# Kernel optimization log

Hardware: AMD Instinct MI355X
Metric: run time of the kernel (lower is better)

Reference implementation:

```python
import jax, jax.numpy as jnp
import numpy as np
from jax import lax

B, S, I, H, L = 128, 256, 64, 128, 64
N_SUB = 2  # fixed RK4 substeps per observation interval (replaces adaptive dopri5)


def setup_inputs() -> dict:
    key = jax.random.key(0)
    ks = jax.random.split(key, 16)
    sc = 0.05
    x = jax.random.normal(ks[0], (B, S, I), jnp.float32)
    # strictly increasing irregular observation times
    times = jnp.sort(jax.random.uniform(ks[1], (S,), jnp.float32) * 10.0)
    return {
        "x": x,
        "times": times,
        "W_ih": jax.random.normal(ks[2], (3 * H, I), jnp.float32) * sc,
        "W_hh": jax.random.normal(ks[3], (3 * H, H), jnp.float32) * sc,
        "b_ih": jnp.zeros((3 * H,), jnp.float32),
        "b_hh": jnp.zeros((3 * H,), jnp.float32),
        "ode_W1": jax.random.normal(ks[4], (H, H), jnp.float32) * sc,
        "ode_b1": jnp.zeros((H,), jnp.float32),
        "ode_W2": jax.random.normal(ks[5], (H, H), jnp.float32) * sc,
        "ode_b2": jnp.zeros((H,), jnp.float32),
        "W_mean": jax.random.normal(ks[6], (L, H), jnp.float32) * sc,
        "b_mean": jnp.zeros((L,), jnp.float32),
        "W_logvar": jax.random.normal(ks[7], (L, H), jnp.float32) * sc,
        "b_logvar": jnp.zeros((L,), jnp.float32),
    }


def reference(x, times, W_ih, W_hh, b_ih, b_hh, ode_W1, ode_b1, ode_W2, ode_b2,
              W_mean, b_mean, W_logvar, b_logvar):
    def ode_f(h):  # MLP dynamics: Linear -> tanh -> Linear (time-independent)
        return jnp.tanh(h @ ode_W1.T + ode_b1) @ ode_W2.T + ode_b2

    def rk4(h, dt):
        k1 = ode_f(h)
        k2 = ode_f(h + 0.5 * dt * k1)
        k3 = ode_f(h + 0.5 * dt * k2)
        k4 = ode_f(h + dt * k3)
        return h + (dt / 6.0) * (k1 + 2.0 * k2 + 2.0 * k3 + k4)

    def gru(x_t, h):  # torch.nn.GRUCell math
        gx = x_t @ W_ih.T + b_ih
        gh = h @ W_hh.T + b_hh
        rx, zx, nx = jnp.split(gx, 3, axis=-1)
        rh, zh, nh = jnp.split(gh, 3, axis=-1)
        r = jax.nn.sigmoid(rx + rh)
        z = jax.nn.sigmoid(zx + zh)
        n = jnp.tanh(nx + r * nh)
        return (1.0 - z) * n + z * h

    # iterate i = S-1 .. 0; before each GRU update (except the first, i=S-1)
    # evolve h from t_{i+1} backward to t_i  -> dt_i = t_i - t_{i+1} (negative)
    dt_rev = jnp.concatenate([jnp.zeros((1,), times.dtype),
                              (times[:-1] - times[1:])[::-1]])  # [S]
    x_rev = jnp.transpose(x[:, ::-1, :], (1, 0, 2))  # [S, B, I]

    def step(h, inp):
        x_t, dt = inp
        sub = dt / N_SUB
        for _ in range(N_SUB):  # fixed small unroll
            h = rk4(h, sub)
        h = gru(x_t, h)
        return h, None

    h0 = jnp.zeros((x.shape[0], W_hh.shape[1]), x.dtype)
    h, _ = lax.scan(step, h0, (x_rev, dt_rev))
    mean = h @ W_mean.T + b_mean
    logvar = h @ W_logvar.T + b_logvar
    return (mean, logvar)
```

## Files before the change

### kernel.cpp

```cpp
#include <hip/hip_runtime.h>

#define NB 128
#define NS 256
#define NI 64
#define NH 128
#define NL 64
#define NG 384

typedef _Float16 f16;
typedef __attribute__((ext_vector_type(2))) _Float16 f16x2;

__device__ __forceinline__ float fast_tanh(float x) {
    float e = __expf(2.0f * x);
    return 1.0f - 2.0f / (e + 1.0f);
}
__device__ __forceinline__ float fast_sig(float x) {
    return 1.0f / (1.0f + __expf(-x));
}
__device__ __forceinline__ float red1(float a) {
    int ai = __builtin_bit_cast(int, a);
    int bi = __builtin_amdgcn_update_dpp(0, ai, 0xB1, 0xF, 0xF, true);
    return a + __builtin_bit_cast(float, bi);
}
__device__ __forceinline__ float fdot2(f16x2 a, f16x2 b, float c) {
#if __has_builtin(__builtin_amdgcn_fdot2)
    return __builtin_amdgcn_fdot2(a, b, c, false);
#else
    return c + (float)a.x * (float)b.x + (float)a.y * (float)b.y;
#endif
}
__device__ __forceinline__ f16x2 bc16(unsigned int u) {
    return __builtin_bit_cast(f16x2, u);
}
__device__ __forceinline__ void sync_lds() {
    asm volatile("s_waitcnt lgkmcnt(0)" ::: "memory");
    __builtin_amdgcn_s_barrier();
    asm volatile("" ::: "memory");
}

__device__ __align__(16) f16 g_W1h[NH * NH];
__device__ __align__(16) f16 g_W2h[NH * NH];
__device__ __align__(16) f16 g_W12h[NH * NH];
__device__ __align__(16) f16 g_Whhh[3 * NH * NH];
__device__ __align__(16) f16 g_Whh2h[3 * NH * NH];
__device__ float g_w1b2[NH];
__device__ float g_whhb2[3 * NH];

__global__ __launch_bounds__(384)
void gx_kernel(const float* __restrict__ x, const float* __restrict__ W_ih,
               const float* __restrict__ b_ih, float* __restrict__ gx)
{
    const int s = blockIdx.x;
    const int j = threadIdx.x;
    __shared__ __align__(16) float xs[NB * NI];
    for (int idx = j; idx < NB * NI; idx += 384) {
        int bb = idx >> 6, cc = idx & 63;
        xs[idx] = x[(bb * NS + s) * NI + cc];
    }
    float w[64];
#pragma unroll
    for (int c = 0; c < 64; c += 4)
        *(float4*)&w[c] = *(const float4*)&W_ih[j * NI + c];
    const float bj = b_ih[j];
    __syncthreads();
    for (int bb = 0; bb < NB; bb++) {
        const float* xr = xs + bb * NI;
        float a0 = 0.f, a1 = 0.f, a2 = 0.f, a3 = 0.f;
#pragma unroll
        for (int c = 0; c < 64; c += 4) {
            a0 = fmaf(w[c + 0], xr[c + 0], a0);
            a1 = fmaf(w[c + 1], xr[c + 1], a1);
            a2 = fmaf(w[c + 2], xr[c + 2], a2);
            a3 = fmaf(w[c + 3], xr[c + 3], a3);
        }
        gx[((size_t)s * NB + bb) * NG + j] = ((a0 + a1) + (a2 + a3)) + bj;
    }
}

__global__ __launch_bounds__(128)
void prep_kernel(const float* __restrict__ W1, const float* __restrict__ Whh,
                 const float* __restrict__ W2, const float* __restrict__ b2)
{
    const int i = blockIdx.x;
    const int j = threadIdx.x;
    __shared__ float rowA[NH];
    __shared__ float red[NH];
    const float* src = (i < NH) ? (W1 + i * NH) : (Whh + (size_t)(i - NH) * NH);
    rowA[j] = src[j];
    __syncthreads();
    float acc = 0.f;
    for (int k = 0; k < NH; k++) acc = fmaf(rowA[k], W2[k * NH + j], acc);
    if (i < NH) {
        g_W12h[i * NH + j] = (f16)acc;
        g_W1h[i * NH + j]  = (f16)rowA[j];
        g_W2h[i * NH + j]  = (f16)W2[i * NH + j];
    } else {
        g_Whh2h[(size_t)(i - NH) * NH + j] = (f16)acc;
        g_Whhh[(size_t)(i - NH) * NH + j]  = (f16)rowA[j];
    }
    red[j] = rowA[j] * b2[j];
    __syncthreads();
    for (int off = 64; off > 0; off >>= 1) {
        if (j < off) red[j] += red[j + off];
        __syncthreads();
    }
    if (j == 0) {
        if (i < NH) g_w1b2[i] = red[0];
        else        g_whhb2[i - NH] = red[0];
    }
}

#define DOT1(W, SRC, OUT)                                                      \
    {                                                                          \
        float a0_ = 0.f, a1_ = 0.f, a2_ = 0.f, a3_ = 0.f;                      \
        _Pragma("unroll") for (int j = 0; j < 8; j++)                          \
        {                                                                      \
            uint4 v_ = *(const uint4*)((const unsigned char*)(SRC) + pbase + 16 * j); \
            a0_ = fdot2(W[4 * j + 0], bc16(v_.x), a0_);                        \
            a1_ = fdot2(W[4 * j + 1], bc16(v_.y), a1_);                        \
            a2_ = fdot2(W[4 * j + 2], bc16(v_.z), a2_);                        \
            a3_ = fdot2(W[4 * j + 3], bc16(v_.w), a3_);                        \
        }                                                                      \
        OUT = red1((a0_ + a1_) + (a2_ + a3_));                                 \
    }

#define DOT2S(WA, WB, SRC, OA, OB)                                             \
    {                                                                          \
        float a0_ = 0.f, a1_ = 0.f, a2_ = 0.f, a3_ = 0.f;                      \
        float b0_ = 0.f, b1_ = 0.f, b2_ = 0.f, b3_ = 0.f;                      \
        _Pragma("unroll") for (int j = 0; j < 8; j++)                          \
        {                                                                      \
            uint4 v_ = *(const uint4*)((const unsigned char*)(SRC) + pbase + 16 * j); \
            a0_ = fdot2(WA[4 * j + 0], bc16(v_.x), a0_);                       \
            a1_ = fdot2(WA[4 * j + 1], bc16(v_.y), a1_);                       \
            a2_ = fdot2(WA[4 * j + 2], bc16(v_.z), a2_);                       \
            a3_ = fdot2(WA[4 * j + 3], bc16(v_.w), a3_);                       \
            b0_ = fdot2(WB[4 * j + 0], bc16(v_.x), b0_);                       \
            b1_ = fdot2(WB[4 * j + 1], bc16(v_.y), b1_);                       \
            b2_ = fdot2(WB[4 * j + 2], bc16(v_.z), b2_);                       \
            b3_ = fdot2(WB[4 * j + 3], bc16(v_.w), b3_);                       \
        }                                                                      \
        OA = red1((a0_ + a1_) + (a2_ + a3_));                                  \
        OB = red1((b0_ + b1_) + (b2_ + b3_));                                  \
    }

#define DOT2D(WA, SA, WB, SB, OA, OB)                                          \
    {                                                                          \
        float a0_ = 0.f, a1_ = 0.f, a2_ = 0.f, a3_ = 0.f;                      \
        float b0_ = 0.f, b1_ = 0.f, b2_ = 0.f, b3_ = 0.f;                      \
        _Pragma("unroll") for (int j = 0; j < 8; j++)                          \
        {                                                                      \
            uint4 v_ = *(const uint4*)((const unsigned char*)(SA) + pbase + 16 * j); \
            uint4 u_ = *(const uint4*)((const unsigned char*)(SB) + pbase + 16 * j); \
            a0_ = fdot2(WA[4 * j + 0], bc16(v_.x), a0_);                       \
            a1_ = fdot2(WA[4 * j + 1], bc16(v_.y), a1_);                       \
            a2_ = fdot2(WA[4 * j + 2], bc16(v_.z), a2_);                       \
            a3_ = fdot2(WA[4 * j + 3], bc16(v_.w), a3_);                       \
            b0_ = fdot2(WB[4 * j + 0], bc16(u_.x), b0_);                       \
            b1_ = fdot2(WB[4 * j + 1], bc16(u_.y), b1_);                       \
            b2_ = fdot2(WB[4 * j + 2], bc16(u_.z), b2_);                       \
            b3_ = fdot2(WB[4 * j + 3], bc16(u_.w), b3_);                       \
        }                                                                      \
        OA = red1((a0_ + a1_) + (a2_ + a3_));                                  \
        OB = red1((b0_ + b1_) + (b2_ + b3_));                                  \
    }

#define DOT4S(WA, WB, WC, WD, SRC, OA, OB, OC, OD)                             \
    {                                                                          \
        float a0_ = 0.f, a1_ = 0.f, b0_ = 0.f, b1_ = 0.f;                      \
        float c0_ = 0.f, c1_ = 0.f, d0_ = 0.f, d1_ = 0.f;                      \
        _Pragma("unroll") for (int j = 0; j < 8; j++)                          \
        {                                                                      \
            uint4 v_ = *(const uint4*)((const unsigned char*)(SRC) + pbase + 16 * j); \
            a0_ = fdot2(WA[4 * j + 0], bc16(v_.x), a0_);                       \
            a1_ = fdot2(WA[4 * j + 1], bc16(v_.y), a1_);                       \
            a0_ = fdot2(WA[4 * j + 2], bc16(v_.z), a0_);                       \
            a1_ = fdot2(WA[4 * j + 3], bc16(v_.w), a1_);                       \
            b0_ = fdot2(WB[4 * j + 0], bc16(v_.x), b0_);                       \
            b1_ = fdot2(WB[4 * j + 1], bc16(v_.y), b1_);                       \
            b0_ = fdot2(WB[4 * j + 2], bc16(v_.z), b0_);                       \
            b1_ = fdot2(WB[4 * j + 3], bc16(v_.w), b1_);                       \
            c0_ = fdot2(WC[4 * j + 0], bc16(v_.x), c0_);                       \
            c1_ = fdot2(WC[4 * j + 1], bc16(v_.y), c1_);                       \
            c0_ = fdot2(WC[4 * j + 2], bc16(v_.z), c0_);                       \
            c1_ = fdot2(WC[4 * j + 3], bc16(v_.w), c1_);                       \
            d0_ = fdot2(WD[4 * j + 0], bc16(v_.x), d0_);                       \
            d1_ = fdot2(WD[4 * j + 1], bc16(v_.y), d1_);                       \
            d0_ = fdot2(WD[4 * j + 2], bc16(v_.z), d0_);                       \
            d1_ = fdot2(WD[4 * j + 3], bc16(v_.w), d1_);                       \
        }                                                                      \
        OA = red1(a0_ + a1_);                                                  \
        OB = red1(b0_ + b1_);                                                  \
        OC = red1(c0_ + c1_);                                                  \
        OD = red1(d0_ + d1_);                                                  \
    }

#define LOADW(DST, BASE)                                                       \
    {                                                                          \
        _Pragma("unroll") for (int j = 0; j < 8; j++)                          \
        {                                                                      \
            uint4 v_ = *(const uint4*)((const unsigned char*)(BASE) + pbase + 16 * j); \
            DST[4 * j + 0] = bc16(v_.x); DST[4 * j + 1] = bc16(v_.y);          \
            DST[4 * j + 2] = bc16(v_.z); DST[4 * j + 3] = bc16(v_.w);          \
        }                                                                      \
    }

__global__ __launch_bounds__(256, 1)
void rnn_kernel(const float* __restrict__ times, const float* __restrict__ b_hh,
                const float* __restrict__ b1, const float* __restrict__ b2,
                const float* __restrict__ W_mean, const float* __restrict__ b_mean,
                const float* __restrict__ W_logvar, const float* __restrict__ b_logvar,
                const float* __restrict__ gx,
                const float* __restrict__ x, const float* __restrict__ W_ih,
                const float* __restrict__ b_ih,
                const int use_gx,
                float* __restrict__ out)
{
    const int b = blockIdx.x;
    const int t = threadIdx.x;
    const int r = t >> 1;
    const int p = t & 1;
    const int pbase = 128 * p;

    __shared__ __align__(16) f16 shHh[NH], shUh[NH], shAh[NH];
    __shared__ float shT[NS];
    __shared__ __align__(16) float shGX[NG], shX[NI], shHf[NH];

    f16x2 w1p[32], w2p[32], w12p[32];
    f16x2 wh0p[32], wh1p[32], wh2p[32];
    f16x2 ws0p[32], ws1p[32], ws2p[32];
    LOADW(w1p,  g_W1h  + r * NH);
    LOADW(w2p,  g_W2h  + r * NH);
    LOADW(w12p, g_W12h + r * NH);
    LOADW(wh0p, g_Whhh + (0 * NH + r) * NH);
    LOADW(wh1p, g_Whhh + (1 * NH + r) * NH);
    LOADW(wh2p, g_Whhh + (2 * NH + r) * NH);
    LOADW(ws0p, g_Whh2h + (size_t)(0 * NH + r) * NH);
    LOADW(ws1p, g_Whh2h + (size_t)(1 * NH + r) * NH);
    LOADW(ws2p, g_Whh2h + (size_t)(2 * NH + r) * NH);

    const float b1r = b1[r], b2r = b2[r];
    const float bh0 = b_hh[r], bh1 = b_hh[NH + r], bh2 = b_hh[2 * NH + r];
    const float w1b2r = g_w1b2[r];
    const float wb0 = g_whhb2[r], wb1 = g_whhb2[NH + r], wb2 = g_whhb2[2 * NH + r];

    if (t < NS) shT[t] = times[t];
    if (t < NH) shHh[t] = (f16)0.f;
    float h = 0.f;
    __syncthreads();

    float gxr = 0.f, gxz = 0.f, gxn = 0.f;
    if (use_gx) {
        const float* g = gx + ((size_t)(NS - 1) * NB + b) * NG;
        gxr = g[r]; gxz = g[NH + r]; gxn = g[2 * NH + r];
    }

    for (int si = 0; si < NS; ++si) {
        const int seq = NS - 1 - si;
        const float dt = (si == 0) ? 0.f : (shT[seq] - shT[seq + 1]);
        const float dts = 0.5f * dt;
        const float a2 = 0.5f * dts;
        const float a6 = dts * (1.f / 6.f);

        float gnr = 0.f, gnz = 0.f, gnn = 0.f;
        if (use_gx) {
            const int seqn = (seq > 0) ? (seq - 1) : 0;
            const float* g = gx + ((size_t)seqn * NB + b) * NG;
            gnr = g[r]; gnz = g[NH + r]; gnn = g[2 * NH + r];
        } else {
            if (t < NI) shX[t] = x[(b * NS + seq) * NI + t];
            __syncthreads();
            for (int idx = t; idx < NG; idx += 256) {
                const float* wr = W_ih + idx * NI;
                float a = 0.f;
#pragma unroll
                for (int cc = 0; cc < NI; cc += 4) {
                    float4 w4 = *(const float4*)(wr + cc);
                    a = fmaf(w4.x, shX[cc + 0], a);
                    a = fmaf(w4.y, shX[cc + 1], a);
                    a = fmaf(w4.z, shX[cc + 2], a);
                    a = fmaf(w4.w, shX[cc + 3], a);
                }
                shGX[idx] = a + b_ih[idx];
            }
            __syncthreads();
        }

        float z1a, u, S, m;
        DOT1(w1p, shHh, z1a);
        z1a += b1r;
        u = fast_tanh(z1a);
        if (p == 0) shUh[r] = (f16)u;
        S = u;
        sync_lds();
        DOT1(w12p, shUh, m);
        u = fast_tanh(z1a + a2 * (m + w1b2r));
        if (p == 0) shUh[r] = (f16)u;
        S += 2.f * u;
        sync_lds();
        DOT1(w12p, shUh, m);
        u = fast_tanh(z1a + a2 * (m + w1b2r));
        if (p == 0) shUh[r] = (f16)u;
        S += 2.f * u;
        sync_lds();
        DOT1(w12p, shUh, m);
        u = fast_tanh(z1a + dts * (m + w1b2r));
        S += u;
        if (p == 0) shUh[r] = (f16)S;
        sync_lds();
        float mA, mB;
        DOT2S(w2p, w12p, shUh, mA, mB);
        const float hA = h + a6 * mA + dts * b2r;
        const float z1b = z1a + a6 * mB + dts * w1b2r;
        u = fast_tanh(z1b);
        if (p == 0) { shAh[r] = (f16)hA; shUh[r] = (f16)u; }
        float S2 = u;
        sync_lds();

        float g0, g1, g2;
        DOT2D(w12p, shUh, wh0p, shAh, m, g0);
        u = fast_tanh(z1b + a2 * (m + w1b2r));
        if (p == 0) shUh[r] = (f16)u;
        S2 += 2.f * u;
        sync_lds();
        DOT2D(w12p, shUh, wh1p, shAh, m, g1);
        u = fast_tanh(z1b + a2 * (m + w1b2r));
        if (p == 0) shUh[r] = (f16)u;
        S2 += 2.f * u;
        sync_lds();
        DOT2D(w12p, shUh, wh2p, shAh, m, g2);
        u = fast_tanh(z1b + dts * (m + w1b2r));
        S2 += u;
        if (p == 0) shUh[r] = (f16)S2;
        sync_lds();
        float n0, n1, n2, n3;
        DOT4S(w2p, ws0p, ws1p, ws2p, shUh, n0, n1, n2, n3);
        const float hB = hA + a6 * n0 + dts * b2r;
        const float rh = g0 + a6 * n1 + dts * wb0 + bh0;
        const float zh = g1 + a6 * n2 + dts * wb1 + bh1;
        const float nh = g2 + a6 * n3 + dts * wb2 + bh2;
        float rx, zx, nx;
        if (use_gx) { rx = gxr; zx = gxz; nx = gxn; }
        else        { rx = shGX[r]; zx = shGX[NH + r]; nx = shGX[2 * NH + r]; }
        const float rr = fast_sig(rx + rh);
        const float zz = fast_sig(zx + zh);
        const float nn = fast_tanh(nx + rr * nh);
        h = (1.f - zz) * nn + zz * hB;
        if (p == 0) shHh[r] = (f16)h;
        gxr = gnr; gxz = gnz; gxn = gnn;
        sync_lds();
    }

    if (p == 0) shHf[r] = h;
    __syncthreads();
    const int sel = r >> 6;
    const int l = r & 63;
    const float* Wf = sel ? W_logvar : W_mean;
    const int hc0 = 64 * p;
    float a0 = 0.f, a1 = 0.f;
#pragma unroll
    for (int jj = 0; jj < 16; jj++) {
        float4 w4 = *(const float4*)&Wf[l * NH + hc0 + 4 * jj];
        float4 h4 = *(const float4*)(shHf + hc0 + 4 * jj);
        a0 = fmaf(w4.x, h4.x, a0);
        a1 = fmaf(w4.y, h4.y, a1);
        a0 = fmaf(w4.z, h4.z, a0);
        a1 = fmaf(w4.w, h4.w, a1);
    }
    float acc = red1(a0 + a1);
    if (p == 0) {
        const float bias = sel ? b_logvar[l] : b_mean[l];
        out[sel * (NB * NL) + b * NL + l] = acc + bias;
    }
}

extern "C" void kernel_launch(void* const* d_in, const int* in_sizes, int n_in,
                              void* d_out, int out_size, void* d_ws, size_t ws_size,
                              hipStream_t stream)
{
    const float* x        = (const float*)d_in[0];
    const float* times    = (const float*)d_in[1];
    const float* W_ih     = (const float*)d_in[2];
    const float* W_hh     = (const float*)d_in[3];
    const float* b_ih     = (const float*)d_in[4];
    const float* b_hh     = (const float*)d_in[5];
    const float* W1       = (const float*)d_in[6];
    const float* b1       = (const float*)d_in[7];
    const float* W2       = (const float*)d_in[8];
    const float* b2       = (const float*)d_in[9];
    const float* W_mean   = (const float*)d_in[10];
    const float* b_mean   = (const float*)d_in[11];
    const float* W_logvar = (const float*)d_in[12];
    const float* b_logvar = (const float*)d_in[13];
    float* out = (float*)d_out;

    float* gxbuf = (float*)d_ws;
    const size_t need = (size_t)NS * NB * NG * sizeof(float);
    const int use_gx = (d_ws != nullptr && ws_size >= need) ? 1 : 0;

    if (use_gx) {
        gx_kernel<<<NS, 384, 0, stream>>>(x, W_ih, b_ih, gxbuf);
    }
    prep_kernel<<<512, 128, 0, stream>>>(W1, W_hh, W2, b2);
    rnn_kernel<<<NB, 256, 0, stream>>>(times, b_hh, b1, b2,
                                       W_mean, b_mean, W_logvar, b_logvar,
                                       gxbuf, x, W_ih, b_ih, use_gx, out);
}
```

Before: 917.8 us.

## Warp-specialize RNN kernel with readlane broadcast matvecs instead of LDS exchanges

Restructures the per-batch recurrent kernel so one wavefront owns the entire ODE MLP chain, with each lane holding two full rows of the weights. The hidden and intermediate vectors are packed as f16 pairs and broadcast through readlane, which removes the LDS writes, barriers and cross-lane reductions between RK4 stages. The other three wavefronts compute the GRU hidden-gate matvecs concurrently, one gate each, and exchange data with the main wave through a few LDS barriers per step. It also always precomputes gx, using a global fallback buffer when the workspace is too small. The cost is much higher register pressure (hundreds of VGPRs per lane) and a serial chain that now runs on a single wave.

```diff
diff --git a/kernel.cpp b/kernel.cpp
--- a/kernel.cpp
+++ b/kernel.cpp
@@ -29,8 +29,12 @@
     return c + (float)a.x * (float)b.x + (float)a.y * (float)b.y;
 #endif
 }
-__device__ __forceinline__ f16x2 bc16(unsigned int u) {
+__device__ __forceinline__ f16x2 bcu(int u) {
     return __builtin_bit_cast(f16x2, u);
+}
+__device__ __forceinline__ int pack2h(float x, float y) {
+    f16x2 v; v.x = (f16)x; v.y = (f16)y;
+    return __builtin_bit_cast(int, v);
 }
 __device__ __forceinline__ void sync_lds() {
     asm volatile("s_waitcnt lgkmcnt(0)" ::: "memory");
@@ -45,6 +49,7 @@
 __device__ __align__(16) f16 g_Whh2h[3 * NH * NH];
 __device__ float g_w1b2[NH];
 __device__ float g_whhb2[3 * NH];
+__device__ float g_gxfb[(size_t)NS * NB * NG];
 
 __global__ __launch_bounds__(384)
 void gx_kernel(const float* __restrict__ x, const float* __restrict__ W_ih,
@@ -110,98 +115,52 @@
     }
 }
 
-#define DOT1(W, SRC, OUT)                                                      \
+#define RL2(WA, WB, PK, OA, OB)                                                \
     {                                                                          \
-        float a0_ = 0.f, a1_ = 0.f, a2_ = 0.f, a3_ = 0.f;                      \
-        _Pragma("unroll") for (int j = 0; j < 8; j++)                          \
+        float a0_ = 0.f, a1_ = 0.f, b0_ = 0.f, b1_ = 0.f;                      \
+        _Pragma("unroll") for (int k = 0; k < 64; k += 2)                      \
         {                                                                      \
-            uint4 v_ = *(const uint4*)((const unsigned char*)(SRC) + pbase + 16 * j); \
-            a0_ = fdot2(W[4 * j + 0], bc16(v_.x), a0_);                        \
-            a1_ = fdot2(W[4 * j + 1], bc16(v_.y), a1_);                        \
-            a2_ = fdot2(W[4 * j + 2], bc16(v_.z), a2_);                        \
-            a3_ = fdot2(W[4 * j + 3], bc16(v_.w), a3_);                        \
+            int s0_ = __builtin_amdgcn_readlane((int)(PK), k);                 \
+            int s1_ = __builtin_amdgcn_readlane((int)(PK), k + 1);             \
+            a0_ = fdot2(WA[k],     bcu(s0_), a0_);                             \
+            b0_ = fdot2(WB[k],     bcu(s0_), b0_);                             \
+            a1_ = fdot2(WA[k + 1], bcu(s1_), a1_);                             \
+            b1_ = fdot2(WB[k + 1], bcu(s1_), b1_);                             \
         }                                                                      \
-        OUT = red1((a0_ + a1_) + (a2_ + a3_));                                 \
-    }
-
-#define DOT2S(WA, WB, SRC, OA, OB)                                             \
-    {                                                                          \
-        float a0_ = 0.f, a1_ = 0.f, a2_ = 0.f, a3_ = 0.f;                      \
-        float b0_ = 0.f, b1_ = 0.f, b2_ = 0.f, b3_ = 0.f;                      \
-        _Pragma("unroll") for (int j = 0; j < 8; j++)                          \
-        {                                                                      \
-            uint4 v_ = *(const uint4*)((const unsigned char*)(SRC) + pbase + 16 * j); \
-            a0_ = fdot2(WA[4 * j + 0], bc16(v_.x), a0_);                       \
-            a1_ = fdot2(WA[4 * j + 1], bc16(v_.y), a1_);                       \
-            a2_ = fdot2(WA[4 * j + 2], bc16(v_.z), a2_);                       \
-            a3_ = fdot2(WA[4 * j + 3], bc16(v_.w), a3_);                       \
-            b0_ = fdot2(WB[4 * j + 0], bc16(v_.x), b0_);                       \
-            b1_ = fdot2(WB[4 * j + 1], bc16(v_.y), b1_);                       \
-            b2_ = fdot2(WB[4 * j + 2], bc16(v_.z), b2_);                       \
-            b3_ = fdot2(WB[4 * j + 3], bc16(v_.w), b3_);                       \
-        }                                                                      \
-        OA = red1((a0_ + a1_) + (a2_ + a3_));                                  \
-        OB = red1((b0_ + b1_) + (b2_ + b3_));                                  \
-    }
-
-#define DOT2D(WA, SA, WB, SB, OA, OB)                                          \
-    {                                                                          \
-        float a0_ = 0.f, a1_ = 0.f, a2_ = 0.f, a3_ = 0.f;                      \
-        float b0_ = 0.f, b1_ = 0.f, b2_ = 0.f, b3_ = 0.f;                      \
-        _Pragma("unroll") for (int j = 0; j < 8; j++)                          \
-        {                                                                      \
-            uint4 v_ = *(const uint4*)((const unsigned char*)(SA) + pbase + 16 * j); \
-            uint4 u_ = *(const uint4*)((const unsigned char*)(SB) + pbase + 16 * j); \
-            a0_ = fdot2(WA[4 * j + 0], bc16(v_.x), a0_);                       \
-            a1_ = fdot2(WA[4 * j + 1], bc16(v_.y), a1_);                       \
-            a2_ = fdot2(WA[4 * j + 2], bc16(v_.z), a2_);                       \
-            a3_ = fdot2(WA[4 * j + 3], bc16(v_.w), a3_);                       \
-            b0_ = fdot2(WB[4 * j + 0], bc16(u_.x), b0_);                       \
-            b1_ = fdot2(WB[4 * j + 1], bc16(u_.y), b1_);                       \
-            b2_ = fdot2(WB[4 * j + 2], bc16(u_.z), b2_);                       \
-            b3_ = fdot2(WB[4 * j + 3], bc16(u_.w), b3_);                       \
-        }                                                                      \
-        OA = red1((a0_ + a1_) + (a2_ + a3_));                                  \
-        OB = red1((b0_ + b1_) + (b2_ + b3_));                                  \
-    }
-
-#define DOT4S(WA, WB, WC, WD, SRC, OA, OB, OC, OD)                             \
+        OA = a0_ + a1_;                                                        \
+        OB = b0_ + b1_;                                                        \
+    }
+
+#define RL4(WA, WB, WC, WD, PK, OA, OB, OC, OD)                                \
     {                                                                          \
         float a0_ = 0.f, a1_ = 0.f, b0_ = 0.f, b1_ = 0.f;                      \
         float c0_ = 0.f, c1_ = 0.f, d0_ = 0.f, d1_ = 0.f;                      \
-        _Pragma("unroll") for (int j = 0; j < 8; j++)                          \
+        _Pragma("unroll") for (int k = 0; k < 64; k += 2)                      \
         {                                                                      \
-            uint4 v_ = *(const uint4*)((const unsigned char*)(SRC) + pbase + 16 * j); \
-            a0_ = fdot2(WA[4 * j + 0], bc16(v_.x), a0_);                       \
-            a1_ = fdot2(WA[4 * j + 1], bc16(v_.y), a1_);                       \
-            a0_ = fdot2(WA[4 * j + 2], bc16(v_.z), a0_);                       \
-            a1_ = fdot2(WA[4 * j + 3], bc16(v_.w), a1_);                       \
-            b0_ = fdot2(WB[4 * j + 0], bc16(v_.x), b0_);                       \
-            b1_ = fdot2(WB[4 * j + 1], bc16(v_.y), b1_);                       \
-            b0_ = fdot2(WB[4 * j + 2], bc16(v_.z), b0_);                       \
-            b1_ = fdot2(WB[4 * j + 3], bc16(v_.w), b1_);                       \
-            c0_ = fdot2(WC[4 * j + 0], bc16(v_.x), c0_);                       \
-            c1_ = fdot2(WC[4 * j + 1], bc16(v_.y), c1_);                       \
-            c0_ = fdot2(WC[4 * j + 2], bc16(v_.z), c0_);                       \
-            c1_ = fdot2(WC[4 * j + 3], bc16(v_.w), c1_);                       \
-            d0_ = fdot2(WD[4 * j + 0], bc16(v_.x), d0_);                       \
-            d1_ = fdot2(WD[4 * j + 1], bc16(v_.y), d1_);                       \
-            d0_ = fdot2(WD[4 * j + 2], bc16(v_.z), d0_);                       \
-            d1_ = fdot2(WD[4 * j + 3], bc16(v_.w), d1_);                       \
+            int s0_ = __builtin_amdgcn_readlane((int)(PK), k);                 \
+            int s1_ = __builtin_amdgcn_readlane((int)(PK), k + 1);             \
+            a0_ = fdot2(WA[k],     bcu(s0_), a0_);                             \
+            b0_ = fdot2(WB[k],     bcu(s0_), b0_);                             \
+            c0_ = fdot2(WC[k],     bcu(s0_), c0_);                             \
+            d0_ = fdot2(WD[k],     bcu(s0_), d0_);                             \
+            a1_ = fdot2(WA[k + 1], bcu(s1_), a1_);                             \
+            b1_ = fdot2(WB[k + 1], bcu(s1_), b1_);                             \
+            c1_ = fdot2(WC[k + 1], bcu(s1_), c1_);                             \
+            d1_ = fdot2(WD[k + 1], bcu(s1_), d1_);                             \
         }                                                                      \
-        OA = red1(a0_ + a1_);                                                  \
-        OB = red1(b0_ + b1_);                                                  \
-        OC = red1(c0_ + c1_);                                                  \
-        OD = red1(d0_ + d1_);                                                  \
-    }
-
-#define LOADW(DST, BASE)                                                       \
+        OA = a0_ + a1_;                                                        \
+        OB = b0_ + b1_;                                                        \
+        OC = c0_ + c1_;                                                        \
+        OD = d0_ + d1_;                                                        \
+    }
+
+#define LOADROW(DST, BASE)                                                     \
     {                                                                          \
-        _Pragma("unroll") for (int j = 0; j < 8; j++)                          \
+        _Pragma("unroll") for (int j = 0; j < 16; j++)                         \
         {                                                                      \
-            uint4 v_ = *(const uint4*)((const unsigned char*)(BASE) + pbase + 16 * j); \
-            DST[4 * j + 0] = bc16(v_.x); DST[4 * j + 1] = bc16(v_.y);          \
-            DST[4 * j + 2] = bc16(v_.z); DST[4 * j + 3] = bc16(v_.w);          \
+            uint4 v_ = *(const uint4*)((const f16*)(BASE) + 8 * j);            \
+            DST[4 * j + 0] = bcu(v_.x); DST[4 * j + 1] = bcu(v_.y);            \
+            DST[4 * j + 2] = bcu(v_.z); DST[4 * j + 3] = bcu(v_.w);            \
         }                                                                      \
     }
 
@@ -211,152 +170,164 @@
                 const float* __restrict__ W_mean, const float* __restrict__ b_mean,
                 const float* __restrict__ W_logvar, const float* __restrict__ b_logvar,
                 const float* __restrict__ gx,
-                const float* __restrict__ x, const float* __restrict__ W_ih,
-                const float* __restrict__ b_ih,
-                const int use_gx,
                 float* __restrict__ out)
 {
     const int b = blockIdx.x;
     const int t = threadIdx.x;
-    const int r = t >> 1;
-    const int p = t & 1;
-    const int pbase = 128 * p;
-
-    __shared__ __align__(16) f16 shHh[NH], shUh[NH], shAh[NH];
+    const int w = t >> 6;
+    const int L = t & 63;
+
     __shared__ float shT[NS];
-    __shared__ __align__(16) float shGX[NG], shX[NI], shHf[NH];
-
-    f16x2 w1p[32], w2p[32], w12p[32];
-    f16x2 wh0p[32], wh1p[32], wh2p[32];
-    f16x2 ws0p[32], ws1p[32], ws2p[32];
-    LOADW(w1p,  g_W1h  + r * NH);
-    LOADW(w2p,  g_W2h  + r * NH);
-    LOADW(w12p, g_W12h + r * NH);
-    LOADW(wh0p, g_Whhh + (0 * NH + r) * NH);
-    LOADW(wh1p, g_Whhh + (1 * NH + r) * NH);
-    LOADW(wh2p, g_Whhh + (2 * NH + r) * NH);
-    LOADW(ws0p, g_Whh2h + (size_t)(0 * NH + r) * NH);
-    LOADW(ws1p, g_Whh2h + (size_t)(1 * NH + r) * NH);
-    LOADW(ws2p, g_Whh2h + (size_t)(2 * NH + r) * NH);
-
-    const float b1r = b1[r], b2r = b2[r];
-    const float bh0 = b_hh[r], bh1 = b_hh[NH + r], bh2 = b_hh[2 * NH + r];
-    const float w1b2r = g_w1b2[r];
-    const float wb0 = g_whhb2[r], wb1 = g_whhb2[NH + r], wb2 = g_whhb2[2 * NH + r];
-
-    if (t < NS) shT[t] = times[t];
-    if (t < NH) shHh[t] = (f16)0.f;
-    float h = 0.f;
-    __syncthreads();
-
-    float gxr = 0.f, gxz = 0.f, gxn = 0.f;
-    if (use_gx) {
-        const float* g = gx + ((size_t)(NS - 1) * NB + b) * NG;
-        gxr = g[r]; gxz = g[NH + r]; gxn = g[2 * NH + r];
-    }
-
-    for (int si = 0; si < NS; ++si) {
-        const int seq = NS - 1 - si;
-        const float dt = (si == 0) ? 0.f : (shT[seq] - shT[seq + 1]);
-        const float dts = 0.5f * dt;
-        const float a2 = 0.5f * dts;
-        const float a6 = dts * (1.f / 6.f);
-
-        float gnr = 0.f, gnz = 0.f, gnn = 0.f;
-        if (use_gx) {
+    __shared__ int shHA[64];
+    __shared__ int shS2[64];
+    __shared__ float2 shG[3][64];
+    __shared__ __align__(16) float shHf[NH];
+
+    for (int i = t; i < NS; i += 256) shT[i] = times[i];
+    __syncthreads();
+
+    if (w == 0) {
+        const int r0 = 2 * L, r1 = 2 * L + 1;
+        f16x2 w1a[64], w1b[64];
+        f16x2 wca[64], wcb[64];
+        f16x2 w2a[64], w2b[64];
+        LOADROW(w1a, g_W1h + r0 * NH); LOADROW(w1b, g_W1h + r1 * NH);
+        LOADROW(wca, g_W12h + r0 * NH); LOADROW(wcb, g_W12h + r1 * NH);
+        LOADROW(w2a, g_W2h + r0 * NH); LOADROW(w2b, g_W2h + r1 * NH);
+        const float b1r0 = b1[r0], b1r1 = b1[r1];
+        const float b2r0 = b2[r0], b2r1 = b2[r1];
+        const float wb0 = g_w1b2[r0], wb1 = g_w1b2[r1];
+
+        float h0 = 0.f, h1 = 0.f;
+        int hpk = 0;
+        const float* gbase = gx + ((size_t)(NS - 1) * NB + b) * NG;
+        float2 gr = *(const float2*)(gbase + r0);
+        float2 gz = *(const float2*)(gbase + NH + r0);
+        float2 gn = *(const float2*)(gbase + 2 * NH + r0);
+
+        for (int si = 0; si < NS; ++si) {
+            const int seq = NS - 1 - si;
+            const float dt = (si == 0) ? 0.f : (shT[seq] - shT[seq + 1]);
+            const float dts = 0.5f * dt;
+            const float a2 = 0.5f * dts;
+            const float a6 = dts * (1.f / 6.f);
+
             const int seqn = (seq > 0) ? (seq - 1) : 0;
-            const float* g = gx + ((size_t)seqn * NB + b) * NG;
-            gnr = g[r]; gnz = g[NH + r]; gnn = g[2 * NH + r];
-        } else {
-            if (t < NI) shX[t] = x[(b * NS + seq) * NI + t];
-            __syncthreads();
-            for (int idx = t; idx < NG; idx += 256) {
-                const float* wr = W_ih + idx * NI;
-                float a = 0.f;
-#pragma unroll
-                for (int cc = 0; cc < NI; cc += 4) {
-                    float4 w4 = *(const float4*)(wr + cc);
-                    a = fmaf(w4.x, shX[cc + 0], a);
-                    a = fmaf(w4.y, shX[cc + 1], a);
-                    a = fmaf(w4.z, shX[cc + 2], a);
-                    a = fmaf(w4.w, shX[cc + 3], a);
-                }
-                shGX[idx] = a + b_ih[idx];
-            }
-            __syncthreads();
+            const float* gb = gx + ((size_t)seqn * NB + b) * NG;
+            float2 gr_n = *(const float2*)(gb + r0);
+            float2 gz_n = *(const float2*)(gb + NH + r0);
+            float2 gn_n = *(const float2*)(gb + 2 * NH + r0);
+
+            float z0, z1v;
+            RL2(w1a, w1b, hpk, z0, z1v);
+            z0 += b1r0; z1v += b1r1;
+            float u0 = fast_tanh(z0), u1 = fast_tanh(z1v);
+            float S0 = u0, S1 = u1;
+            int upk = pack2h(u0, u1);
+            float m0, m1;
+            RL2(wca, wcb, upk, m0, m1);
+            u0 = fast_tanh(z0 + a2 * (m0 + wb0));
+            u1 = fast_tanh(z1v + a2 * (m1 + wb1));
+            S0 += 2.f * u0; S1 += 2.f * u1;
+            upk = pack2h(u0, u1);
+            RL2(wca, wcb, upk, m0, m1);
+            u0 = fast_tanh(z0 + a2 * (m0 + wb0));
+            u1 = fast_tanh(z1v + a2 * (m1 + wb1));
+            S0 += 2.f * u0; S1 += 2.f * u1;
+            upk = pack2h(u0, u1);
+            RL2(wca, wcb, upk, m0, m1);
+            u0 = fast_tanh(z0 + dts * (m0 + wb0));
+            u1 = fast_tanh(z1v + dts * (m1 + wb1));
+            S0 += u0; S1 += u1;
+            int Spk = pack2h(S0, S1);
+            float mA0, mA1, mW0, mW1;
+            RL4(wca, wcb, w2a, w2b, Spk, mA0, mA1, mW0, mW1);
+            const float zb0 = z0 + a6 * mA0 + dts * wb0;
+            const float zb1 = z1v + a6 * mA1 + dts * wb1;
+            const float hA0 = h0 + a6 * mW0 + dts * b2r0;
+            const float hA1 = h1 + a6 * mW1 + dts * b2r1;
+            shHA[L] = pack2h(hA0, hA1);
+            u0 = fast_tanh(zb0); u1 = fast_tanh(zb1);
+            float S20 = u0, S21 = u1;
+            upk = pack2h(u0, u1);
+            sync_lds();
+            RL2(wca, wcb, upk, m0, m1);
+            u0 = fast_tanh(zb0 + a2 * (m0 + wb0));
+            u1 = fast_tanh(zb1 + a2 * (m1 + wb1));
+            S20 += 2.f * u0; S21 += 2.f * u1;
+            upk = pack2h(u0, u1);
+            RL2(wca, wcb, upk, m0, m1);
+            u0 = fast_tanh(zb0 + a2 * (m0 + wb0));
+            u1 = fast_tanh(zb1 + a2 * (m1 + wb1));
+            S20 += 2.f * u0; S21 += 2.f * u1;
+            upk = pack2h(u0, u1);
+            RL2(wca, wcb, upk, m0, m1);
+            u0 = fast_tanh(zb0 + dts * (m0 + wb0));
+            u1 = fast_tanh(zb1 + dts * (m1 + wb1));
+            S20 += u0; S21 += u1;
+            int S2pk = pack2h(S20, S21);
+            shS2[L] = S2pk;
+            sync_lds();
+            float n0, n1;
+            RL2(w2a, w2b, S2pk, n0, n1);
+            const float hB0 = hA0 + a6 * n0 + dts * b2r0;
+            const float hB1 = hA1 + a6 * n1 + dts * b2r1;
+            sync_lds();
+            float2 Gr = shG[0][L];
+            float2 Gz = shG[1][L];
+            float2 Gn = shG[2][L];
+            const float rr0 = fast_sig(gr.x + Gr.x);
+            const float rr1 = fast_sig(gr.y + Gr.y);
+            const float zz0 = fast_sig(gz.x + Gz.x);
+            const float zz1 = fast_sig(gz.y + Gz.y);
+            const float nn0 = fast_tanh(gn.x + rr0 * Gn.x);
+            const float nn1 = fast_tanh(gn.y + rr1 * Gn.y);
+            h0 = (1.f - zz0) * nn0 + zz0 * hB0;
+            h1 = (1.f - zz1) * nn1 + zz1 * hB1;
+            hpk = pack2h(h0, h1);
+            gr = gr_n; gz = gz_n; gn = gn_n;
         }
-
-        float z1a, u, S, m;
-        DOT1(w1p, shHh, z1a);
-        z1a += b1r;
-        u = fast_tanh(z1a);
-        if (p == 0) shUh[r] = (f16)u;
-        S = u;
-        sync_lds();
-        DOT1(w12p, shUh, m);
-        u = fast_tanh(z1a + a2 * (m + w1b2r));
-        if (p == 0) shUh[r] = (f16)u;
-        S += 2.f * u;
-        sync_lds();
-        DOT1(w12p, shUh, m);
-        u = fast_tanh(z1a + a2 * (m + w1b2r));
-        if (p == 0) shUh[r] = (f16)u;
-        S += 2.f * u;
-        sync_lds();
-        DOT1(w12p, shUh, m);
-        u = fast_tanh(z1a + dts * (m + w1b2r));
-        S += u;
-        if (p == 0) shUh[r] = (f16)S;
-        sync_lds();
-        float mA, mB;
-        DOT2S(w2p, w12p, shUh, mA, mB);
-        const float hA = h + a6 * mA + dts * b2r;
-        const float z1b = z1a + a6 * mB + dts * w1b2r;
-        u = fast_tanh(z1b);
-        if (p == 0) { shAh[r] = (f16)hA; shUh[r] = (f16)u; }
-        float S2 = u;
-        sync_lds();
-
-        float g0, g1, g2;
-        DOT2D(w12p, shUh, wh0p, shAh, m, g0);
-        u = fast_tanh(z1b + a2 * (m + w1b2r));
-        if (p == 0) shUh[r] = (f16)u;
-        S2 += 2.f * u;
-        sync_lds();
-        DOT2D(w12p, shUh, wh1p, shAh, m, g1);
-        u = fast_tanh(z1b + a2 * (m + w1b2r));
-        if (p == 0) shUh[r] = (f16)u;
-        S2 += 2.f * u;
-        sync_lds();
-        DOT2D(w12p, shUh, wh2p, shAh, m, g2);
-        u = fast_tanh(z1b + dts * (m + w1b2r));
-        S2 += u;
-        if (p == 0) shUh[r] = (f16)S2;
-        sync_lds();
-        float n0, n1, n2, n3;
-        DOT4S(w2p, ws0p, ws1p, ws2p, shUh, n0, n1, n2, n3);
-        const float hB = hA + a6 * n0 + dts * b2r;
-        const float rh = g0 + a6 * n1 + dts * wb0 + bh0;
-        const float zh = g1 + a6 * n2 + dts * wb1 + bh1;
-        const float nh = g2 + a6 * n3 + dts * wb2 + bh2;
-        float rx, zx, nx;
-        if (use_gx) { rx = gxr; zx = gxz; nx = gxn; }
-        else        { rx = shGX[r]; zx = shGX[NH + r]; nx = shGX[2 * NH + r]; }
-        const float rr = fast_sig(rx + rh);
-        const float zz = fast_sig(zx + zh);
-        const float nn = fast_tanh(nx + rr * nh);
-        h = (1.f - zz) * nn + zz * hB;
-        if (p == 0) shHh[r] = (f16)h;
-        gxr = gnr; gxz = gnz; gxn = gnn;
-        sync_lds();
-    }
-
-    if (p == 0) shHf[r] = h;
-    __syncthreads();
-    const int sel = r >> 6;
-    const int l = r & 63;
+        shHf[r0] = h0;
+        shHf[r1] = h1;
+    } else {
+        const int g = w - 1;
+        const int r0 = 2 * L, r1 = 2 * L + 1;
+        f16x2 wha[64], whb[64];
+        f16x2 wsa[64], wsb[64];
+        LOADROW(wha, g_Whhh + (size_t)(g * NH + r0) * NH);
+        LOADROW(whb, g_Whhh + (size_t)(g * NH + r1) * NH);
+        LOADROW(wsa, g_Whh2h + (size_t)(g * NH + r0) * NH);
+        LOADROW(wsb, g_Whh2h + (size_t)(g * NH + r1) * NH);
+        const float bh0 = b_hh[g * NH + r0], bh1 = b_hh[g * NH + r1];
+        const float sb0 = g_whhb2[g * NH + r0], sb1 = g_whhb2[g * NH + r1];
+
+        for (int si = 0; si < NS; ++si) {
+            const int seq = NS - 1 - si;
+            const float dt = (si == 0) ? 0.f : (shT[seq] - shT[seq + 1]);
+            const float dts = 0.5f * dt;
+            const float a6 = dts * (1.f / 6.f);
+
+            sync_lds();
+            int hApk = shHA[L];
+            float gA0, gA1;
+            RL2(wha, whb, hApk, gA0, gA1);
+            sync_lds();
+            int S2pk = shS2[L];
+            float gS0, gS1;
+            RL2(wsa, wsb, S2pk, gS0, gS1);
+            shG[g][L] = make_float2(gA0 + a6 * gS0 + dts * sb0 + bh0,
+                                    gA1 + a6 * gS1 + dts * sb1 + bh1);
+            sync_lds();
+        }
+    }
+
+    __syncthreads();
+    const int rr = t >> 1;
+    const int pp = t & 1;
+    const int sel = rr >> 6;
+    const int l = rr & 63;
     const float* Wf = sel ? W_logvar : W_mean;
-    const int hc0 = 64 * p;
+    const int hc0 = 64 * pp;
     float a0 = 0.f, a1 = 0.f;
 #pragma unroll
     for (int jj = 0; jj < 16; jj++) {
@@ -368,7 +339,7 @@
         a1 = fmaf(w4.w, h4.w, a1);
     }
     float acc = red1(a0 + a1);
-    if (p == 0) {
+    if (pp == 0) {
         const float bias = sel ? b_logvar[l] : b_mean[l];
         out[sel * (NB * NL) + b * NL + l] = acc + bias;
     }
@@ -394,15 +365,19 @@
     const float* b_logvar = (const float*)d_in[13];
     float* out = (float*)d_out;
 
-    float* gxbuf = (float*)d_ws;
     const size_t need = (size_t)NS * NB * NG * sizeof(float);
-    const int use_gx = (d_ws != nullptr && ws_size >= need) ? 1 : 0;
-
-    if (use_gx) {
-        gx_kernel<<<NS, 384, 0, stream>>>(x, W_ih, b_ih, gxbuf);
-    }
+    float* gxbuf;
+    if (d_ws != nullptr && ws_size >= need) {
+        gxbuf = (float*)d_ws;
+    } else {
+        void* p = nullptr;
+        hipGetSymbolAddress(&p, HIP_SYMBOL(g_gxfb));
+        gxbuf = (float*)p;
+    }
+
+    gx_kernel<<<NS, 384, 0, stream>>>(x, W_ih, b_ih, gxbuf);
     prep_kernel<<<512, 128, 0, stream>>>(W1, W_hh, W2, b2);
     rnn_kernel<<<NB, 256, 0, stream>>>(times, b_hh, b1, b2,
                                        W_mean, b_mean, W_logvar, b_logvar,
-                                       gxbuf, x, W_ih, b_ih, use_gx, out);
-}
+                                       gxbuf, out);
+}
```

Measured after the change: 1.719 ms. 1.87x slower.
